# Kernel optimization log

Measured on AMD Instinct MI355X. Metric: run time of the kernel, lower is better.

The kernel has to match this reference:

```python
import jax, jax.numpy as jnp
import numpy as np

B, S, H, HD, WIN, KS = 2, 2048, 8, 64, 64, 2048
D = H * HD          # slotsize = nheads * headsize = 512
SUB = 1 + 2 * WIN   # window length = 129
LN_EPS = 1e-3       # Keras LayerNormalization default epsilon


def setup_inputs() -> dict:
    key = jax.random.key(0)
    ks = jax.random.split(key, 5)
    s = 0.02
    return {
        "values": jax.random.normal(ks[0], (B, S, D), jnp.float32),
        "W_kqv": jax.random.normal(ks[1], (D, 3 * D), jnp.float32) * s,
        "b_kqv": jnp.zeros((3 * D,), jnp.float32),
        "ln_gamma": jnp.ones((D,), jnp.float32),
        "ln_beta": jnp.zeros((D,), jnp.float32),
        "W_kernel": jax.random.normal(ks[2], (D, KS), jnp.float32) * s,
        "b_kernel": jnp.zeros((KS,), jnp.float32),
        "W_proj": jax.random.normal(ks[3], (KS, D), jnp.float32) * s,
        "b_proj": jnp.zeros((D,), jnp.float32),
    }


def _layernorm(x, g, b):
    mu = jnp.mean(x, axis=-1, keepdims=True)
    var = jnp.var(x, axis=-1, keepdims=True)
    return (x - mu) * jax.lax.rsqrt(var + LN_EPS) * g + b


def reference(values, W_kqv, b_kqv, ln_gamma, ln_beta, W_kernel, b_kernel, W_proj, b_proj):
    # fused qkv projection: [B,S,3D]
    kqv = values @ W_kqv + b_kqv
    k, q, v = jnp.split(kqv, 3, axis=2)
    # shared layernorm applied to q and k (over full D)
    q = _layernorm(q, ln_gamma, ln_beta)
    k = _layernorm(k, ln_gamma, ln_beta)
    kh = k.reshape(B, S, H, HD)
    qh = q.reshape(B, S, H, HD)
    vh = v.reshape(B, S, H, HD)
    starts = jnp.clip(jnp.arange(S) - WIN, 0, S - SUB)
    idx = starts[:, None] + jnp.arange(SUB)          # [S, SUB]
    kw = kh[:, idx]                                  # [B,S,SUB,H,HD]
    vw = vh[:, idx]                                  # [B,S,SUB,H,HD]
    scores = jnp.einsum('bshd,bswhd->bshw', qh, kw) / np.float32(np.sqrt(HD))
    attn = jax.nn.softmax(scores, axis=-1)           # [B,S,H,SUB]
    ctx = jnp.einsum('bshw,bswhd->bshd', attn, vw).reshape(B, S, D)
    # residual MLP (dropout rate 0 -> identity)
    x = jax.nn.relu(ctx @ W_kernel + b_kernel)
    x = x @ W_proj + b_proj
    return x + v  # residual is the value projection, per the original code
```

## Files before the change

kernel.cpp:

```cpp
#include <hip/hip_runtime.h>
#include <hip/hip_bf16.h>

#define B_ 2
#define S_ 2048
#define H_ 8
#define HD_ 64
#define WIN_ 64
#define SUB_ 129
#define D_ 512
#define KS_ 2048
#define M_ 4096
#define LN_EPS 1e-3f

typedef unsigned short u16;
typedef short bf16x8 __attribute__((ext_vector_type(8)));
typedef float f32x4 __attribute__((ext_vector_type(4)));

__device__ inline u16 f2bf(float x) {
  unsigned int u = __float_as_uint(x);
  return (u16)((u + 0x7fffu + ((u >> 16) & 1u)) >> 16);
}
__device__ inline float bf2f(u16 u) {
  return __uint_as_float(((unsigned int)u) << 16);
}
__device__ inline float bf2f_lo(unsigned int u) { return __uint_as_float(u << 16); }
__device__ inline float bf2f_hi(unsigned int u) { return __uint_as_float(u & 0xffff0000u); }

__device__ inline void gll16(const u16* g, u16* l) {
  __builtin_amdgcn_global_load_lds(
      (const __attribute__((address_space(1))) void*)g,
      (__attribute__((address_space(3))) void*)l, 16, 0, 0);
}

template <int EPI>
__global__ __launch_bounds__(256) void mfma_gemm(
    const u16* __restrict__ A, const u16* __restrict__ Bt,
    const float* __restrict__ bias, u16* __restrict__ Cout, int K, int lda,
    int ldb, int ldc, int TN) {
  __shared__ __align__(16) u16 As[2][8192];
  __shared__ __align__(16) u16 Bs[2][8192];

  const int tid = threadIdx.x;
  const int wv = tid >> 6;
  const int ln = tid & 63;

  const int id = blockIdx.x;
  const int xcd = id & 7;
  const int sub = id >> 3;
  const int tn = sub % TN;
  const int msub = sub / TN;
  const int row0 = (xcd * 4 + msub) << 7;
  const int col0 = tn << 7;

  const int lrow = ln >> 3;
  const int lchunk = (ln & 7) ^ lrow;
  const u16* ag = A + (size_t)(row0 + 32 * wv + lrow) * lda + lchunk * 8;
  const u16* bg = Bt + (size_t)(col0 + 32 * wv + lrow) * ldb + lchunk * 8;
  const int lbase = 32 * wv * 64;

  const int q = ln >> 4;
  const int r16 = ln & 15;
  const int r8 = r16 & 7;
  const int wm = (wv & 1) << 6;
  const int wn = (wv >> 1) << 6;

  f32x4 acc[4][4];
#pragma unroll
  for (int i = 0; i < 4; ++i)
#pragma unroll
    for (int j = 0; j < 4; ++j) acc[i][j] = (f32x4){0.f, 0.f, 0.f, 0.f};

#define STAGE(buf, koff)                                            \
  do {                                                              \
    const u16* a0 = ag + (koff);                                    \
    const u16* b0 = bg + (koff);                                    \
    u16* la = &As[buf][lbase];                                      \
    u16* lb = &Bs[buf][lbase];                                      \
    gll16(a0, la);                                                  \
    gll16(a0 + 8 * (size_t)lda, la + 512);                          \
    gll16(a0 + 16 * (size_t)lda, la + 1024);                        \
    gll16(a0 + 24 * (size_t)lda, la + 1536);                        \
    gll16(b0, lb);                                                  \
    gll16(b0 + 8 * (size_t)ldb, lb + 512);                          \
    gll16(b0 + 16 * (size_t)ldb, lb + 1024);                        \
    gll16(b0 + 24 * (size_t)ldb, lb + 1536);                        \
  } while (0)

  const int nk = K >> 6;
  STAGE(0, 0);

  for (int ki = 0; ki < nk; ++ki) {
    __syncthreads();
    if (ki + 1 < nk) STAGE((ki + 1) & 1, (ki + 1) << 6);

    const char* Ab = (const char*)As[ki & 1];
    const char* Bb = (const char*)Bs[ki & 1];
#pragma unroll
    for (int ks = 0; ks < 2; ++ks) {
      const int pc = ((q + 4 * ks) ^ r8) << 4;
      bf16x8 af[4], bfv[4];
#pragma unroll
      for (int mi = 0; mi < 4; ++mi)
        af[mi] = *(const bf16x8*)(Ab + (wm + 16 * mi + r16) * 128 + pc);
#pragma unroll
      for (int ni = 0; ni < 4; ++ni)
        bfv[ni] = *(const bf16x8*)(Bb + (wn + 16 * ni + r16) * 128 + pc);
#pragma unroll
      for (int mi = 0; mi < 4; ++mi)
#pragma unroll
        for (int ni = 0; ni < 4; ++ni)
          acc[mi][ni] = __builtin_amdgcn_mfma_f32_16x16x32_bf16(
              af[mi], bfv[ni], acc[mi][ni], 0, 0, 0);
    }
  }
#undef STAGE

  const int colb = col0 + wn + r16;
  float bv[4];
#pragma unroll
  for (int ni = 0; ni < 4; ++ni) bv[ni] = bias[colb + ni * 16];

#pragma unroll
  for (int mi = 0; mi < 4; ++mi) {
#pragma unroll
    for (int ni = 0; ni < 4; ++ni) {
      const int col = colb + ni * 16;
#pragma unroll
      for (int r = 0; r < 4; ++r) {
        const int row = row0 + wm + mi * 16 + (q << 2) + r;
        float v = acc[mi][ni][r] + bv[ni];
        if (EPI == 1) v = fmaxf(v, 0.f);
        Cout[(size_t)row * ldc + col] = f2bf(v);
      }
    }
  }
}

__global__ __launch_bounds__(256) void mfma_gemm64(
    const u16* __restrict__ A, const u16* __restrict__ Bt,
    const float* __restrict__ bias, const u16* __restrict__ extra,
    float* __restrict__ Cout, int K, int lda, int ldb, int ldc, int eld,
    int TN, int MB) {
  __shared__ __align__(16) u16 As[2][4096];
  __shared__ __align__(16) u16 Bs[2][8192];

  const int tid = threadIdx.x;
  const int wv = tid >> 6;
  const int ln = tid & 63;

  const int id = blockIdx.x;
  const int xcd = id & 7;
  const int sub = id >> 3;
  const int tn = sub % TN;
  const int msub = sub / TN;
  const int row0 = (xcd * MB + msub) << 6;
  const int col0 = tn << 7;

  const int lrow = ln >> 3;
  const int lchunk = (ln & 7) ^ lrow;
  const u16* ag = A + (size_t)(row0 + 16 * wv + lrow) * lda + lchunk * 8;
  const u16* bg = Bt + (size_t)(col0 + 32 * wv + lrow) * ldb + lchunk * 8;

  const int q = ln >> 4;
  const int r16 = ln & 15;
  const int r8 = r16 & 7;
  const int wn = wv << 5;

  f32x4 acc[4][2];
#pragma unroll
  for (int i = 0; i < 4; ++i)
#pragma unroll
    for (int j = 0; j < 2; ++j) acc[i][j] = (f32x4){0.f, 0.f, 0.f, 0.f};

#define STAGE64(buf, koff)                                          \
  do {                                                              \
    const u16* a0 = ag + (koff);                                    \
    const u16* b0 = bg + (koff);                                    \
    u16* la = &As[buf][wv * 1024];                                  \
    u16* lb = &Bs[buf][wv * 2048];                                  \
    gll16(a0, la);                                                  \
    gll16(a0 + 8 * (size_t)lda, la + 512);                          \
    gll16(b0, lb);                                                  \
    gll16(b0 + 8 * (size_t)ldb, lb + 512);                          \
    gll16(b0 + 16 * (size_t)ldb, lb + 1024);                        \
    gll16(b0 + 24 * (size_t)ldb, lb + 1536);                        \
  } while (0)

  const int nk = K >> 6;
  STAGE64(0, 0);

  for (int ki = 0; ki < nk; ++ki) {
    __syncthreads();
    if (ki + 1 < nk) STAGE64((ki + 1) & 1, (ki + 1) << 6);

    const char* Ab = (const char*)As[ki & 1];
    const char* Bb = (const char*)Bs[ki & 1];
#pragma unroll
    for (int ks = 0; ks < 2; ++ks) {
      const int pc = ((q + 4 * ks) ^ r8) << 4;
      bf16x8 af[4], bfv[2];
#pragma unroll
      for (int mi = 0; mi < 4; ++mi)
        af[mi] = *(const bf16x8*)(Ab + (16 * mi + r16) * 128 + pc);
#pragma unroll
      for (int ni = 0; ni < 2; ++ni)
        bfv[ni] = *(const bf16x8*)(Bb + (wn + 16 * ni + r16) * 128 + pc);
#pragma unroll
      for (int mi = 0; mi < 4; ++mi)
#pragma unroll
        for (int ni = 0; ni < 2; ++ni)
          acc[mi][ni] = __builtin_amdgcn_mfma_f32_16x16x32_bf16(
              af[mi], bfv[ni], acc[mi][ni], 0, 0, 0);
    }
  }
#undef STAGE64

  const int colb = col0 + wn + r16;
  float bv[2];
#pragma unroll
  for (int ni = 0; ni < 2; ++ni) bv[ni] = bias[colb + ni * 16];

#pragma unroll
  for (int mi = 0; mi < 4; ++mi) {
#pragma unroll
    for (int ni = 0; ni < 2; ++ni) {
      const int col = colb + ni * 16;
#pragma unroll
      for (int r = 0; r < 4; ++r) {
        const int row = row0 + mi * 16 + (q << 2) + r;
        Cout[(size_t)row * ldc + col] =
            acc[mi][ni][r] + bv[ni] + bf2f(extra[(size_t)row * eld + col]);
      }
    }
  }
}

__global__ __launch_bounds__(256) void cvt_kernel(const float* __restrict__ in,
                                                  u16* __restrict__ out) {
  const int i = (blockIdx.x * 256 + threadIdx.x) * 8;
  float4 a = *(const float4*)&in[i];
  float4 b = *(const float4*)&in[i + 4];
  union { u16 u[8]; uint4 v; } pk;
  pk.u[0] = f2bf(a.x); pk.u[1] = f2bf(a.y); pk.u[2] = f2bf(a.z); pk.u[3] = f2bf(a.w);
  pk.u[4] = f2bf(b.x); pk.u[5] = f2bf(b.y); pk.u[6] = f2bf(b.z); pk.u[7] = f2bf(b.w);
  *(uint4*)&out[i] = pk.v;
}

__global__ __launch_bounds__(256) void cvtT_kernel(const float* __restrict__ W,
                                                   u16* __restrict__ Wt, int K,
                                                   int N) {
  __shared__ float t[32][33];
  const int n0 = blockIdx.x << 5;
  const int k0 = blockIdx.y << 5;
  const int r = threadIdx.x >> 3;
  const int c4 = (threadIdx.x & 7) << 2;
  float4 v = *(const float4*)&W[(size_t)(k0 + r) * N + n0 + c4];
  t[r][c4 + 0] = v.x; t[r][c4 + 1] = v.y; t[r][c4 + 2] = v.z; t[r][c4 + 3] = v.w;
  __syncthreads();
  ushort4 o;
  o.x = f2bf(t[c4 + 0][r]); o.y = f2bf(t[c4 + 1][r]);
  o.z = f2bf(t[c4 + 2][r]); o.w = f2bf(t[c4 + 3][r]);
  *(ushort4*)&Wt[(size_t)(n0 + r) * K + k0 + c4] = o;
}

__global__ __launch_bounds__(128) void ln_kernel(u16* __restrict__ kqv,
                                                 const float* __restrict__ gamma,
                                                 const float* __restrict__ beta) {
  const int row = blockIdx.x;
  const int bs = row >> 1;
  const int which = row & 1;
  u16* p = kqv + (size_t)bs * 1536 + (which ? 512 : 0);
  const int tid = threadIdx.x;
  const int c = tid << 2;

  uint2 raw = *(uint2*)&p[c];
  float x0 = bf2f_lo(raw.x), x1 = bf2f_hi(raw.x);
  float x2 = bf2f_lo(raw.y), x3 = bf2f_hi(raw.y);
  float s = x0 + x1 + x2 + x3;
  float ss = x0 * x0 + x1 * x1 + x2 * x2 + x3 * x3;

#pragma unroll
  for (int off = 32; off > 0; off >>= 1) {
    s += __shfl_down(s, off);
    ss += __shfl_down(ss, off);
  }
  __shared__ float red[4];
  if ((tid & 63) == 0) {
    red[(tid >> 6) * 2 + 0] = s;
    red[(tid >> 6) * 2 + 1] = ss;
  }
  __syncthreads();
  const float tot = red[0] + red[2];
  const float tots = red[1] + red[3];
  const float mean = tot * (1.f / 512.f);
  const float var = tots * (1.f / 512.f) - mean * mean;
  const float rstd = rsqrtf(var + LN_EPS);

  float4 g = *(const float4*)&gamma[c];
  float4 bb = *(const float4*)&beta[c];
  union { u16 u[4]; uint2 v; } o;
  o.u[0] = f2bf((x0 - mean) * rstd * g.x + bb.x);
  o.u[1] = f2bf((x1 - mean) * rstd * g.y + bb.y);
  o.u[2] = f2bf((x2 - mean) * rstd * g.z + bb.z);
  o.u[3] = f2bf((x3 - mean) * rstd * g.w + bb.w);
  *(uint2*)&p[c] = o.v;
}

__global__ __launch_bounds__(256) void attn_kernel(const u16* __restrict__ kqv,
                                                   u16* __restrict__ ctx) {
  __shared__ __align__(16) u16 Ks[192 * 64];
  __shared__ __align__(16) u16 Vt[64 * 192];
  __shared__ __align__(16) u16 Ps[4 * 16 * 192];

  const int bid = blockIdx.x;
  const int tile = bid & 31;
  const int h = (bid >> 5) & 7;
  const int b = bid >> 8;
  const int t0 = tile << 6;

  int g0 = t0 - WIN_;
  if (g0 < 0) g0 = 0;
  if (g0 > S_ - SUB_) g0 = S_ - SUB_;

  const int tid = threadIdx.x;
  const size_t rowb = (size_t)(b * S_);

#pragma unroll
  for (int it = 0; it < 6; ++it) {
    const int item = tid + it * 256;
    const int key = item >> 3, c = item & 7;
    const int phys = c ^ (key & 7);
    uint4 v = *(const uint4*)&kqv[(rowb + g0 + key) * 1536 + h * 64 + c * 8];
    *(uint4*)&Ks[key * 64 + phys * 8] = v;
  }
#pragma unroll
  for (int it = 0; it < 2; ++it) {
    const int item = tid + it * 256;
    const int qq = item >> 3, c = item & 7;
    const int phys = c ^ (qq & 7);
    uint4 v = *(const uint4*)&kqv[(rowb + t0 + qq) * 1536 + 512 + h * 64 + c * 8];
    *(uint4*)&Ps[qq * 64 + phys * 8] = v;
  }
#pragma unroll
  for (int it = 0; it < 12; ++it) {
    const int item = tid + it * 256;
    const int dg = item >> 7 == 0 ? item / 192 : item / 192;
    const int key = item - dg * 192;
    uint2 v = *(const uint2*)&kqv[(rowb + g0 + key) * 1536 + 1024 + h * 64 + dg * 4];
    const int c = key >> 3;
    u16 e[4] = {(u16)(v.x & 0xffff), (u16)(v.x >> 16),
                (u16)(v.y & 0xffff), (u16)(v.y >> 16)};
#pragma unroll
    for (int j = 0; j < 4; ++j) {
      const int d = dg * 4 + j;
      const int phys = (c & 24) | ((c ^ d) & 7);
      Vt[d * 192 + phys * 8 + (key & 7)] = e[j];
    }
  }
  __syncthreads();

  const int wv = tid >> 6;
  const int ln = tid & 63;
  const int quad = ln >> 4;
  const int l15 = ln & 15;
  const int l7 = l15 & 7;
  const int qbase = wv << 4;

  bf16x8 qf[2];
#pragma unroll
  for (int ks = 0; ks < 2; ++ks) {
    const int phys = (ks * 4 + quad) ^ l7;
    qf[ks] = *(const bf16x8*)&Ps[(qbase + l15) * 64 + phys * 8];
  }

  f32x4 sacc[12];
#pragma unroll
  for (int nt = 0; nt < 12; ++nt) sacc[nt] = (f32x4){0.f, 0.f, 0.f, 0.f};
#pragma unroll
  for (int ks = 0; ks < 2; ++ks) {
    const int phys = (ks * 4 + quad) ^ l7;
#pragma unroll
    for (int nt = 0; nt < 12; ++nt) {
      bf16x8 kf = *(const bf16x8*)&Ks[(nt * 16 + l15) * 64 + phys * 8];
      sacc[nt] = __builtin_amdgcn_mfma_f32_16x16x32_bf16(qf[ks], kf, sacc[nt], 0, 0, 0);
    }
  }

  int off[4];
#pragma unroll
  for (int r = 0; r < 4; ++r) {
    const int qg = t0 + qbase + quad * 4 + r;
    int st = qg - WIN_;
    if (st < 0) st = 0;
    if (st > S_ - SUB_) st = S_ - SUB_;
    off[r] = st - g0;
  }

  float rmax[4] = {-1e30f, -1e30f, -1e30f, -1e30f};
#pragma unroll
  for (int nt = 0; nt < 12; ++nt) {
    const int n = nt * 16 + l15;
#pragma unroll
    for (int r = 0; r < 4; ++r) {
      const bool valid = (n >= off[r]) && (n < off[r] + SUB_);
      const float v = valid ? sacc[nt][r] * 0.125f : -1e30f;
      sacc[nt][r] = v;
      rmax[r] = fmaxf(rmax[r], v);
    }
  }
#pragma unroll
  for (int m = 1; m < 16; m <<= 1)
#pragma unroll
    for (int r = 0; r < 4; ++r) rmax[r] = fmaxf(rmax[r], __shfl_xor(rmax[r], m));

  float rsum[4] = {0.f, 0.f, 0.f, 0.f};
#pragma unroll
  for (int nt = 0; nt < 12; ++nt) {
#pragma unroll
    for (int r = 0; r < 4; ++r) {
      const float e = __expf(sacc[nt][r] - rmax[r]);
      sacc[nt][r] = e;
      rsum[r] += e;
    }
  }
#pragma unroll
  for (int m = 1; m < 16; m <<= 1)
#pragma unroll
    for (int r = 0; r < 4; ++r) rsum[r] += __shfl_xor(rsum[r], m);
  float inv[4];
#pragma unroll
  for (int r = 0; r < 4; ++r) inv[r] = 1.f / rsum[r];

  __syncthreads();

  u16* psw = &Ps[wv * 16 * 192];
#pragma unroll
  for (int nt = 0; nt < 12; ++nt) {
    const int n = nt * 16 + l15;
    const int c = n >> 3;
#pragma unroll
    for (int r = 0; r < 4; ++r) {
      const int m = quad * 4 + r;
      const int phys = (c & 24) | ((c ^ m) & 7);
      psw[m * 192 + phys * 8 + (n & 7)] = f2bf(sacc[nt][r]);
    }
  }
  __syncthreads();

  f32x4 oacc[4];
#pragma unroll
  for (int nt = 0; nt < 4; ++nt) oacc[nt] = (f32x4){0.f, 0.f, 0.f, 0.f};
#pragma unroll
  for (int ks = 0; ks < 6; ++ks) {
    const int c = ks * 4 + quad;
    const int phys = (c & 24) | ((c ^ l7) & 7);
    bf16x8 pf = *(const bf16x8*)&psw[l15 * 192 + phys * 8];
#pragma unroll
    for (int nt = 0; nt < 4; ++nt) {
      bf16x8 vf = *(const bf16x8*)&Vt[(nt * 16 + l15) * 192 + phys * 8];
      oacc[nt] = __builtin_amdgcn_mfma_f32_16x16x32_bf16(pf, vf, oacc[nt], 0, 0, 0);
    }
  }

#pragma unroll
  for (int nt = 0; nt < 4; ++nt) {
#pragma unroll
    for (int r = 0; r < 4; ++r) {
      const int row = t0 + qbase + quad * 4 + r;
      const int col = h * 64 + nt * 16 + l15;
      ctx[(rowb + row) * D_ + col] = f2bf(oacc[nt][r] * inv[r]);
    }
  }
}

extern "C" void kernel_launch(void* const* d_in, const int* in_sizes, int n_in,
                              void* d_out, int out_size, void* d_ws,
                              size_t ws_size, hipStream_t stream) {
  (void)in_sizes; (void)n_in; (void)out_size; (void)ws_size;
  const float* values   = (const float*)d_in[0];
  const float* W_kqv    = (const float*)d_in[1];
  const float* b_kqv    = (const float*)d_in[2];
  const float* ln_gamma = (const float*)d_in[3];
  const float* ln_beta  = (const float*)d_in[4];
  const float* W_kernel = (const float*)d_in[5];
  const float* b_kernel = (const float*)d_in[6];
  const float* W_proj   = (const float*)d_in[7];
  const float* b_proj   = (const float*)d_in[8];
  float* out = (float*)d_out;

  u16* kqv     = (u16*)d_ws;
  u16* vals_bf = kqv + (size_t)M_ * 1536;
  u16* ctx_bf  = vals_bf + (size_t)M_ * 512;
  u16* x_bf    = ctx_bf + (size_t)M_ * 512;
  u16* wkqv_t  = x_bf + (size_t)M_ * 2048;
  u16* wker_t  = wkqv_t + (size_t)1536 * 512;
  u16* wproj_t = wker_t + (size_t)2048 * 512;

  cvt_kernel<<<(M_ * 512) / 2048, 256, 0, stream>>>(values, vals_bf);
  cvtT_kernel<<<dim3(1536 / 32, 512 / 32), 256, 0, stream>>>(W_kqv, wkqv_t, 512, 1536);
  cvtT_kernel<<<dim3(2048 / 32, 512 / 32), 256, 0, stream>>>(W_kernel, wker_t, 512, 2048);
  cvtT_kernel<<<dim3(512 / 32, 2048 / 32), 256, 0, stream>>>(W_proj, wproj_t, 2048, 512);

  mfma_gemm<3><<<384, 256, 0, stream>>>(
      vals_bf, wkqv_t, b_kqv, kqv, 512, 512, 512, 1536, 12);

  ln_kernel<<<2 * M_, 128, 0, stream>>>(kqv, ln_gamma, ln_beta);

  attn_kernel<<<B_ * H_ * (S_ / 64), 256, 0, stream>>>(kqv, ctx_bf);

  mfma_gemm<1><<<512, 256, 0, stream>>>(
      ctx_bf, wker_t, b_kernel, x_bf, 512, 512, 512, KS_, 16);

  mfma_gemm64<<<256, 256, 0, stream>>>(
      x_bf, wproj_t, b_proj, kqv + 1024, out, KS_, KS_, KS_, D_, 1536, 4, 8);
}
```

Before: 159.1 us.

## Halve GEMM K-tile to 32 and swap MFMA operands for vectorized epilogue

Both MFMA GEMM kernels now stage K-tiles of 32 instead of 64, halving LDS use, with a new 4-chunk XOR swizzle and a single MFMA step per tile. The MFMA operands are swapped so each lane holds four consecutive output columns, letting the epilogue use float4 bias loads, vector residual loads and vector stores instead of scalar ones. The smaller LDS footprint may raise occupancy, but it doubles the number of barriers and loop iterations per unit of K.

```diff
diff --git a/kernel.cpp b/kernel.cpp
--- a/kernel.cpp
+++ b/kernel.cpp
@@ -37,8 +37,8 @@
     const u16* __restrict__ A, const u16* __restrict__ Bt,
     const float* __restrict__ bias, u16* __restrict__ Cout, int K, int lda,
     int ldb, int ldc, int TN) {
-  __shared__ __align__(16) u16 As[2][8192];
-  __shared__ __align__(16) u16 Bs[2][8192];
+  __shared__ __align__(16) u16 As[2][4096];
+  __shared__ __align__(16) u16 Bs[2][4096];
 
   const int tid = threadIdx.x;
   const int wv = tid >> 6;
@@ -52,15 +52,15 @@
   const int row0 = (xcd * 4 + msub) << 7;
   const int col0 = tn << 7;
 
-  const int lrow = ln >> 3;
-  const int lchunk = (ln & 7) ^ lrow;
+  const int lrow = ln >> 2;
+  const int lchunk = (ln & 3) ^ ((ln >> 3) & 3);
   const u16* ag = A + (size_t)(row0 + 32 * wv + lrow) * lda + lchunk * 8;
   const u16* bg = Bt + (size_t)(col0 + 32 * wv + lrow) * ldb + lchunk * 8;
-  const int lbase = 32 * wv * 64;
-
-  const int q = ln >> 4;
-  const int r16 = ln & 15;
-  const int r8 = r16 & 7;
+  const int lbase = wv * 1024;
+
+  const int quad = ln >> 4;
+  const int l15 = ln & 15;
+  const int pc = (quad ^ ((l15 >> 1) & 3)) << 4;
   const int wm = (wv & 1) << 6;
   const int wn = (wv >> 1) << 6;
 
@@ -72,66 +72,57 @@
 
 #define STAGE(buf, koff)                                            \
   do {                                                              \
-    const u16* a0 = ag + (koff);                                    \
-    const u16* b0 = bg + (koff);                                    \
-    u16* la = &As[buf][lbase];                                      \
-    u16* lb = &Bs[buf][lbase];                                      \
-    gll16(a0, la);                                                  \
-    gll16(a0 + 8 * (size_t)lda, la + 512);                          \
-    gll16(a0 + 16 * (size_t)lda, la + 1024);                        \
-    gll16(a0 + 24 * (size_t)lda, la + 1536);                        \
-    gll16(b0, lb);                                                  \
-    gll16(b0 + 8 * (size_t)ldb, lb + 512);                          \
-    gll16(b0 + 16 * (size_t)ldb, lb + 1024);                        \
-    gll16(b0 + 24 * (size_t)ldb, lb + 1536);                        \
+    gll16(ag + (koff), &As[buf][lbase]);                            \
+    gll16(ag + (koff) + 16 * (size_t)lda, &As[buf][lbase + 512]);   \
+    gll16(bg + (koff), &Bs[buf][lbase]);                            \
+    gll16(bg + (koff) + 16 * (size_t)ldb, &Bs[buf][lbase + 512]);   \
   } while (0)
 
-  const int nk = K >> 6;
+  const int nk = K >> 5;
   STAGE(0, 0);
 
   for (int ki = 0; ki < nk; ++ki) {
     __syncthreads();
-    if (ki + 1 < nk) STAGE((ki + 1) & 1, (ki + 1) << 6);
+    if (ki + 1 < nk) STAGE((ki + 1) & 1, (ki + 1) << 5);
 
     const char* Ab = (const char*)As[ki & 1];
     const char* Bb = (const char*)Bs[ki & 1];
-#pragma unroll
-    for (int ks = 0; ks < 2; ++ks) {
-      const int pc = ((q + 4 * ks) ^ r8) << 4;
-      bf16x8 af[4], bfv[4];
-#pragma unroll
-      for (int mi = 0; mi < 4; ++mi)
-        af[mi] = *(const bf16x8*)(Ab + (wm + 16 * mi + r16) * 128 + pc);
+    bf16x8 af[4], bfv[4];
+#pragma unroll
+    for (int mi = 0; mi < 4; ++mi)
+      af[mi] = *(const bf16x8*)(Ab + (wm + 16 * mi + l15) * 64 + pc);
+#pragma unroll
+    for (int ni = 0; ni < 4; ++ni)
+      bfv[ni] = *(const bf16x8*)(Bb + (wn + 16 * ni + l15) * 64 + pc);
+#pragma unroll
+    for (int mi = 0; mi < 4; ++mi)
 #pragma unroll
       for (int ni = 0; ni < 4; ++ni)
-        bfv[ni] = *(const bf16x8*)(Bb + (wn + 16 * ni + r16) * 128 + pc);
-#pragma unroll
-      for (int mi = 0; mi < 4; ++mi)
-#pragma unroll
-        for (int ni = 0; ni < 4; ++ni)
-          acc[mi][ni] = __builtin_amdgcn_mfma_f32_16x16x32_bf16(
-              af[mi], bfv[ni], acc[mi][ni], 0, 0, 0);
-    }
+        acc[mi][ni] = __builtin_amdgcn_mfma_f32_16x16x32_bf16(
+            bfv[ni], af[mi], acc[mi][ni], 0, 0, 0);
   }
 #undef STAGE
 
-  const int colb = col0 + wn + r16;
-  float bv[4];
-#pragma unroll
-  for (int ni = 0; ni < 4; ++ni) bv[ni] = bias[colb + ni * 16];
+  const int c00 = col0 + wn + (quad << 2);
+  float4 bv[4];
+#pragma unroll
+  for (int ni = 0; ni < 4; ++ni) bv[ni] = *(const float4*)&bias[c00 + ni * 16];
 
 #pragma unroll
   for (int mi = 0; mi < 4; ++mi) {
+    const int row = row0 + wm + 16 * mi + l15;
 #pragma unroll
     for (int ni = 0; ni < 4; ++ni) {
-      const int col = colb + ni * 16;
-#pragma unroll
-      for (int r = 0; r < 4; ++r) {
-        const int row = row0 + wm + mi * 16 + (q << 2) + r;
-        float v = acc[mi][ni][r] + bv[ni];
-        if (EPI == 1) v = fmaxf(v, 0.f);
-        Cout[(size_t)row * ldc + col] = f2bf(v);
+      float v0 = acc[mi][ni][0] + bv[ni].x;
+      float v1 = acc[mi][ni][1] + bv[ni].y;
+      float v2 = acc[mi][ni][2] + bv[ni].z;
+      float v3 = acc[mi][ni][3] + bv[ni].w;
+      if (EPI == 1) {
+        v0 = fmaxf(v0, 0.f); v1 = fmaxf(v1, 0.f);
+        v2 = fmaxf(v2, 0.f); v3 = fmaxf(v3, 0.f);
       }
+      ushort4 o = {f2bf(v0), f2bf(v1), f2bf(v2), f2bf(v3)};
+      *(ushort4*)&Cout[(size_t)row * ldc + c00 + ni * 16] = o;
     }
   }
 }
@@ -141,8 +132,8 @@
     const float* __restrict__ bias, const u16* __restrict__ extra,
     float* __restrict__ Cout, int K, int lda, int ldb, int ldc, int eld,
     int TN, int MB) {
-  __shared__ __align__(16) u16 As[2][4096];
-  __shared__ __align__(16) u16 Bs[2][8192];
+  __shared__ __align__(16) u16 As[2][2048];
+  __shared__ __align__(16) u16 Bs[2][4096];
 
   const int tid = threadIdx.x;
   const int wv = tid >> 6;
@@ -156,14 +147,16 @@
   const int row0 = (xcd * MB + msub) << 6;
   const int col0 = tn << 7;
 
-  const int lrow = ln >> 3;
-  const int lchunk = (ln & 7) ^ lrow;
+  const int lrow = ln >> 2;
+  const int lchunk = (ln & 3) ^ ((ln >> 3) & 3);
   const u16* ag = A + (size_t)(row0 + 16 * wv + lrow) * lda + lchunk * 8;
   const u16* bg = Bt + (size_t)(col0 + 32 * wv + lrow) * ldb + lchunk * 8;
-
-  const int q = ln >> 4;
-  const int r16 = ln & 15;
-  const int r8 = r16 & 7;
+  const int abase = wv * 512;
+  const int bbase = wv * 1024;
+
+  const int quad = ln >> 4;
+  const int l15 = ln & 15;
+  const int pc = (quad ^ ((l15 >> 1) & 3)) << 4;
   const int wn = wv << 5;
 
   f32x4 acc[4][2];
@@ -174,63 +167,54 @@
 
 #define STAGE64(buf, koff)                                          \
   do {                                                              \
-    const u16* a0 = ag + (koff);                                    \
-    const u16* b0 = bg + (koff);                                    \
-    u16* la = &As[buf][wv * 1024];                                  \
-    u16* lb = &Bs[buf][wv * 2048];                                  \
-    gll16(a0, la);                                                  \
-    gll16(a0 + 8 * (size_t)lda, la + 512);                          \
-    gll16(b0, lb);                                                  \
-    gll16(b0 + 8 * (size_t)ldb, lb + 512);                          \
-    gll16(b0 + 16 * (size_t)ldb, lb + 1024);                        \
-    gll16(b0 + 24 * (size_t)ldb, lb + 1536);                        \
+    gll16(ag + (koff), &As[buf][abase]);                            \
+    gll16(bg + (koff), &Bs[buf][bbase]);                            \
+    gll16(bg + (koff) + 16 * (size_t)ldb, &Bs[buf][bbase + 512]);   \
   } while (0)
 
-  const int nk = K >> 6;
+  const int nk = K >> 5;
   STAGE64(0, 0);
 
   for (int ki = 0; ki < nk; ++ki) {
     __syncthreads();
-    if (ki + 1 < nk) STAGE64((ki + 1) & 1, (ki + 1) << 6);
+    if (ki + 1 < nk) STAGE64((ki + 1) & 1, (ki + 1) << 5);
 
     const char* Ab = (const char*)As[ki & 1];
     const char* Bb = (const char*)Bs[ki & 1];
-#pragma unroll
-    for (int ks = 0; ks < 2; ++ks) {
-      const int pc = ((q + 4 * ks) ^ r8) << 4;
-      bf16x8 af[4], bfv[2];
-#pragma unroll
-      for (int mi = 0; mi < 4; ++mi)
-        af[mi] = *(const bf16x8*)(Ab + (16 * mi + r16) * 128 + pc);
+    bf16x8 af[4], bfv[2];
+#pragma unroll
+    for (int mi = 0; mi < 4; ++mi)
+      af[mi] = *(const bf16x8*)(Ab + (16 * mi + l15) * 64 + pc);
+#pragma unroll
+    for (int ni = 0; ni < 2; ++ni)
+      bfv[ni] = *(const bf16x8*)(Bb + (wn + 16 * ni + l15) * 64 + pc);
+#pragma unroll
+    for (int mi = 0; mi < 4; ++mi)
 #pragma unroll
       for (int ni = 0; ni < 2; ++ni)
-        bfv[ni] = *(const bf16x8*)(Bb + (wn + 16 * ni + r16) * 128 + pc);
-#pragma unroll
-      for (int mi = 0; mi < 4; ++mi)
-#pragma unroll
-        for (int ni = 0; ni < 2; ++ni)
-          acc[mi][ni] = __builtin_amdgcn_mfma_f32_16x16x32_bf16(
-              af[mi], bfv[ni], acc[mi][ni], 0, 0, 0);
-    }
+        acc[mi][ni] = __builtin_amdgcn_mfma_f32_16x16x32_bf16(
+            bfv[ni], af[mi], acc[mi][ni], 0, 0, 0);
   }
 #undef STAGE64
 
-  const int colb = col0 + wn + r16;
-  float bv[2];
-#pragma unroll
-  for (int ni = 0; ni < 2; ++ni) bv[ni] = bias[colb + ni * 16];
+  const int c00 = col0 + wn + (quad << 2);
+  float4 bv[2];
+#pragma unroll
+  for (int ni = 0; ni < 2; ++ni) bv[ni] = *(const float4*)&bias[c00 + ni * 16];
 
 #pragma unroll
   for (int mi = 0; mi < 4; ++mi) {
+    const int row = row0 + 16 * mi + l15;
 #pragma unroll
     for (int ni = 0; ni < 2; ++ni) {
-      const int col = colb + ni * 16;
-#pragma unroll
-      for (int r = 0; r < 4; ++r) {
-        const int row = row0 + mi * 16 + (q << 2) + r;
-        Cout[(size_t)row * ldc + col] =
-            acc[mi][ni][r] + bv[ni] + bf2f(extra[(size_t)row * eld + col]);
-      }
+      const int c = c00 + ni * 16;
+      uint2 ex = *(const uint2*)&extra[(size_t)row * eld + c];
+      float4 o;
+      o.x = acc[mi][ni][0] + bv[ni].x + bf2f_lo(ex.x);
+      o.y = acc[mi][ni][1] + bv[ni].y + bf2f_hi(ex.x);
+      o.z = acc[mi][ni][2] + bv[ni].z + bf2f_lo(ex.y);
+      o.w = acc[mi][ni][3] + bv[ni].w + bf2f_hi(ex.y);
+      *(float4*)&Cout[(size_t)row * ldc + c] = o;
     }
   }
 }
@@ -344,7 +328,7 @@
 #pragma unroll
   for (int it = 0; it < 12; ++it) {
     const int item = tid + it * 256;
-    const int dg = item >> 7 == 0 ? item / 192 : item / 192;
+    const int dg = item / 192;
     const int key = item - dg * 192;
     uint2 v = *(const uint2*)&kqv[(rowb + g0 + key) * 1536 + 1024 + h * 64 + dg * 4];
     const int c = key >> 3;
```

Result: slower. 172.7 us (+8.6%).
